# Kernel optimization log

Measured on AMD Instinct MI355X. Metric: run time of the kernel, lower is better.

## Reference

```python
import jax, jax.numpy as jnp
import numpy as np

BS = 16     # block_size
KS = 2      # kernel_size
ST = 2      # stride
TOL = 0.5   # mask threshold (avgpool=False -> max-pool reduce)


def setup_inputs() -> dict:
    key = jax.random.key(0)
    k1, k2, k3, k4 = jax.random.split(key, 4)
    inputs = jax.random.normal(k1, (8, 256, 256, 64), dtype=jnp.float32)
    mask = jax.random.uniform(k2, (8, 256, 256, 1), dtype=jnp.float32)
    # TF conv2d_transpose filter layout: [kh, kw, out_channels(filters), in_channels]
    kernel = jax.random.normal(k3, (KS, KS, 64, 64), dtype=jnp.float32) * 0.05
    bias = jax.random.normal(k4, (64,), dtype=jnp.float32) * 0.05
    return {"inputs": inputs, "mask": mask, "kernel": kernel, "bias": bias}


def reference(inputs, mask, kernel, bias):
    N, H, W, C = inputs.shape
    kh, kw, F, _ = kernel.shape
    nbh, nbw = H // BS, W // BS           # block_count
    obs = (BS - 1) * ST + kh              # output_block_size (VALID deconv of a block) = 32

    # sparse.reduce_mask: max-pool mask over each 16x16 block, threshold at tol.
    active = mask.reshape(N, nbh, BS, nbw, BS, -1).max(axis=(2, 4, 5)) > TOL  # [N, nbh, nbw]

    # sparse.gather: extract all blocks (inactive ones are masked out after the conv,
    # which reproduces scatter-into-zeros of only the active blocks).
    blocks = (inputs.reshape(N, nbh, BS, nbw, BS, C)
              .transpose(0, 1, 3, 2, 4, 5)
              .reshape(N * nbh * nbw, BS, BS, C))

    # tf.nn.conv2d_transpose (VALID, stride ST) == dilated conv with rot180 kernel.
    # kernel [kh,kw,out,in] -> HWIO [kh,kw,in,out], spatially flipped.
    w = kernel.transpose(0, 1, 3, 2)[::-1, ::-1]
    out = jax.lax.conv_general_dilated(
        blocks, w,
        window_strides=(1, 1),
        padding=[(kh - 1, kh - 1), (kw - 1, kw - 1)],
        lhs_dilation=(ST, ST),
        dimension_numbers=('NHWC', 'HWIO', 'NHWC'))  # [NB, obs, obs, F]

    out = out + bias  # bias_add; activation is identity (activation=None)

    # sparse.scatter: write active blocks into zero output (non-overlapping tiling).
    out = out.reshape(N, nbh, nbw, obs, obs, F)
    out = out * active[:, :, :, None, None, None].astype(out.dtype)
    out = out.transpose(0, 1, 3, 2, 4, 5).reshape(N, nbh * obs, nbw * obs, F)
    return out  # [N, H*ST, W*ST, F]
```

## Files before the change

### kernel.cpp

```cpp
#include <hip/hip_runtime.h>
#include <hip/hip_bf16.h>

typedef __attribute__((ext_vector_type(4))) float f32x4;
typedef __attribute__((ext_vector_type(8))) short s16x8;

__device__ inline unsigned cvtpk(float a, float b) {
  unsigned r;
  asm("v_cvt_pk_bf16_f32 %0, %1, %2" : "=v"(r) : "v"(a), "v"(b));
  return r;
}
__device__ inline s16x8 pack8(f32x4 a, f32x4 b) {
  union { unsigned u[4]; s16x8 v; } x;
  x.u[0] = cvtpk(a[0], a[1]); x.u[1] = cvtpk(a[2], a[3]);
  x.u[2] = cvtpk(b[0], b[1]); x.u[3] = cvtpk(b[2], b[3]);
  return x.v;
}

__device__ inline void lds_fence() {
  asm volatile("s_waitcnt lgkmcnt(0)" ::: "memory");
  __builtin_amdgcn_sched_barrier(0);
}

__global__ __launch_bounds__(256, 3)
void sparse_deconv_kernel(const float* __restrict__ in, const float* __restrict__ mask,
                          const float* __restrict__ kern, const float* __restrict__ bias,
                          float* __restrict__ out) {
  __shared__ float lds[4][2][2048];
  const int tid = threadIdx.x;
  const int w  = tid >> 6;
  const int l  = tid & 63;
  const int lm = l & 15;
  const int lg = l >> 4;
  const int r  = w & 1;
  const int ky = w >> 1;

  s16x8 wf[8][2];
#pragma unroll
  for (int m2 = 0; m2 < 8; ++m2) {
#pragma unroll
    for (int kf = 0; kf < 2; ++kf) {
      const float* p = kern + (((ky * 8 + m2) * 16 + lm) * 64 + kf * 32 + lg * 8);
      wf[m2][kf] = pack8(*(const f32x4*)p, *(const f32x4*)(p + 4));
    }
  }
  const f32x4 bias4 = *(const f32x4*)(bias + lm * 4);

  const int b  = blockIdx.x;
  const int n  = b >> 8;
  const int by = (b >> 4) & 15;
  const int bx = b & 15;

  const float* mp = mask + ((n * 256 + by * 16) * 256 + bx * 16);
  float mv = 0.0f;
#pragma unroll
  for (int i = 0; i < 4; ++i) {
    const int idx = i * 64 + l;
    mv = fmaxf(mv, mp[(idx >> 4) * 256 + (idx & 15)]);
  }
#pragma unroll
  for (int off = 32; off; off >>= 1)
    mv = fmaxf(mv, __shfl_xor(mv, off));
  const bool active = mv > 0.5f;

  const float* ibase = in + (((n * 256 + by * 16) * 256) + bx * 16 + lm) * 64 + lg * 8;
  float* oorigin = out + (((size_t)(n * 512 + by * 32)) * 512 + bx * 32) * 64;
  const int oyw = 2 * r + ky;

  if (active) {
    f32x4 tb[2][4];
#pragma unroll
    for (int q = 0; q < 2; ++q) {
      const float* p = ibase + (2 * q + r) * (256 * 64);
      tb[q][0] = *(const f32x4*)p;        tb[q][1] = *(const f32x4*)(p + 4);
      tb[q][2] = *(const f32x4*)(p + 32); tb[q][3] = *(const f32x4*)(p + 36);
    }
#pragma unroll
    for (int s = 0; s < 8; ++s) {
      const int bsel = s & 1;
      s16x8 xf0 = pack8(tb[bsel][0], tb[bsel][1]);
      s16x8 xf1 = pack8(tb[bsel][2], tb[bsel][3]);
      if (s < 6) {
        const float* p = ibase + (2 * (s + 2) + r) * (256 * 64);
        tb[bsel][0] = *(const f32x4*)p;        tb[bsel][1] = *(const f32x4*)(p + 4);
        tb[bsel][2] = *(const f32x4*)(p + 32); tb[bsel][3] = *(const f32x4*)(p + 36);
      }
      float* LB = &lds[w][bsel][0];
#pragma unroll
      for (int kx = 0; kx < 2; ++kx) {
#pragma unroll
        for (int ft = 0; ft < 4; ++ft) {
          f32x4 acc = {0.f, 0.f, 0.f, 0.f};
          acc = __builtin_amdgcn_mfma_f32_16x16x32_bf16(wf[kx * 4 + ft][0], xf0, acc, 0, 0, 0);
          acc = __builtin_amdgcn_mfma_f32_16x16x32_bf16(wf[kx * 4 + ft][1], xf1, acc, 0, 0, 0);
          const int p  = 2 * lm + kx;
          const int sl = (4 * ft + lg + p) & 15;
          *(f32x4*)(LB + p * 64 + sl * 4) = acc;
        }
      }
      lds_fence();

      const int oy = 4 * s + oyw;
      float* orow = oorigin + (size_t)oy * (512 * 64) + l * 4;
#pragma unroll
      for (int rc = 0; rc < 8; ++rc) {
        const int p  = rc * 4 + lg;
        const int sl = (lm + p) & 15;
        f32x4 v = *(const f32x4*)(LB + p * 64 + sl * 4);
        v += bias4;
        __builtin_nontemporal_store(v, (f32x4*)(orow + rc * 256));
      }
    }
  } else {
    const f32x4 z = {0.f, 0.f, 0.f, 0.f};
#pragma unroll
    for (int i = 0; i < 8; ++i) {
      float* orow = oorigin + (size_t)(w * 8 + i) * (512 * 64) + l * 4;
#pragma unroll
      for (int rc = 0; rc < 8; ++rc)
        __builtin_nontemporal_store(z, (f32x4*)(orow + rc * 256));
    }
  }
}

extern "C" void kernel_launch(void* const* d_in, const int* in_sizes, int n_in,
                              void* d_out, int out_size, void* d_ws, size_t ws_size,
                              hipStream_t stream) {
  const float* in   = (const float*)d_in[0];
  const float* mask = (const float*)d_in[1];
  const float* kern = (const float*)d_in[2];
  const float* bias = (const float*)d_in[3];
  float* out = (float*)d_out;
  dim3 grid(2048), block(256);
  hipLaunchKernelGGL(sparse_deconv_kernel, grid, block, 0, stream,
                     in, mask, kern, bias, out);
}
```

Measured before the change: 132.0 us.

## Give each wave both kernel rows to read each input row only once

```diff
diff --git a/kernel.cpp b/kernel.cpp
--- a/kernel.cpp
+++ b/kernel.cpp
@@ -21,7 +21,7 @@
   __builtin_amdgcn_sched_barrier(0);
 }
 
-__global__ __launch_bounds__(256, 3)
+__global__ __launch_bounds__(256, 2)
 void sparse_deconv_kernel(const float* __restrict__ in, const float* __restrict__ mask,
                           const float* __restrict__ kern, const float* __restrict__ bias,
                           float* __restrict__ out) {
@@ -31,18 +31,15 @@
   const int l  = tid & 63;
   const int lm = l & 15;
   const int lg = l >> 4;
-  const int r  = w & 1;
-  const int ky = w >> 1;
 
-  s16x8 wf[8][2];
+  s16x8 wf[16][2];
 #pragma unroll
-  for (int m2 = 0; m2 < 8; ++m2) {
+  for (int mt = 0; mt < 16; ++mt)
 #pragma unroll
     for (int kf = 0; kf < 2; ++kf) {
-      const float* p = kern + (((ky * 8 + m2) * 16 + lm) * 64 + kf * 32 + lg * 8);
-      wf[m2][kf] = pack8(*(const f32x4*)p, *(const f32x4*)(p + 4));
+      const float* p = kern + ((mt * 16 + lm) * 64 + kf * 32 + lg * 8);
+      wf[mt][kf] = pack8(*(const f32x4*)p, *(const f32x4*)(p + 4));
     }
-  }
   const f32x4 bias4 = *(const f32x4*)(bias + lm * 4);
 
   const int b  = blockIdx.x;
@@ -62,63 +59,67 @@
     mv = fmaxf(mv, __shfl_xor(mv, off));
   const bool active = mv > 0.5f;
 
-  const float* ibase = in + (((n * 256 + by * 16) * 256) + bx * 16 + lm) * 64 + lg * 8;
+  const float* ibase = in + (((n * 256 + by * 16 + w) * 256) + bx * 16 + lm) * 64 + lg * 8;
   float* oorigin = out + (((size_t)(n * 512 + by * 32)) * 512 + bx * 32) * 64;
-  const int oyw = 2 * r + ky;
 
   if (active) {
     f32x4 tb[2][4];
 #pragma unroll
     for (int q = 0; q < 2; ++q) {
-      const float* p = ibase + (2 * q + r) * (256 * 64);
+      const float* p = ibase + (4 * q) * (256 * 64);
       tb[q][0] = *(const f32x4*)p;        tb[q][1] = *(const f32x4*)(p + 4);
       tb[q][2] = *(const f32x4*)(p + 32); tb[q][3] = *(const f32x4*)(p + 36);
     }
 #pragma unroll
-    for (int s = 0; s < 8; ++s) {
+    for (int s = 0; s < 4; ++s) {
       const int bsel = s & 1;
       s16x8 xf0 = pack8(tb[bsel][0], tb[bsel][1]);
       s16x8 xf1 = pack8(tb[bsel][2], tb[bsel][3]);
-      if (s < 6) {
-        const float* p = ibase + (2 * (s + 2) + r) * (256 * 64);
+      if (s < 2) {
+        const float* p = ibase + (4 * (s + 2)) * (256 * 64);
         tb[bsel][0] = *(const f32x4*)p;        tb[bsel][1] = *(const f32x4*)(p + 4);
         tb[bsel][2] = *(const f32x4*)(p + 32); tb[bsel][3] = *(const f32x4*)(p + 36);
       }
-      float* LB = &lds[w][bsel][0];
 #pragma unroll
-      for (int kx = 0; kx < 2; ++kx) {
+      for (int ky = 0; ky < 2; ++ky) {
+        float* LB = &lds[w][ky][0];
 #pragma unroll
-        for (int ft = 0; ft < 4; ++ft) {
-          f32x4 acc = {0.f, 0.f, 0.f, 0.f};
-          acc = __builtin_amdgcn_mfma_f32_16x16x32_bf16(wf[kx * 4 + ft][0], xf0, acc, 0, 0, 0);
-          acc = __builtin_amdgcn_mfma_f32_16x16x32_bf16(wf[kx * 4 + ft][1], xf1, acc, 0, 0, 0);
-          const int p  = 2 * lm + kx;
-          const int sl = (4 * ft + lg + p) & 15;
-          *(f32x4*)(LB + p * 64 + sl * 4) = acc;
+        for (int kx = 0; kx < 2; ++kx)
+#pragma unroll
+          for (int ft = 0; ft < 4; ++ft) {
+            f32x4 acc = {0.f, 0.f, 0.f, 0.f};
+            acc = __builtin_amdgcn_mfma_f32_16x16x32_bf16(wf[ky * 8 + kx * 4 + ft][0], xf0, acc, 0, 0, 0);
+            acc = __builtin_amdgcn_mfma_f32_16x16x32_bf16(wf[ky * 8 + kx * 4 + ft][1], xf1, acc, 0, 0, 0);
+            const int p  = 2 * lm + kx;
+            const int sl = (4 * ft + lg + p) & 15;
+            *(f32x4*)(LB + p * 64 + sl * 4) = acc;
+          }
+        lds_fence();
+
+        const int oy = 8 * s + 2 * w + ky;
+        float* orow = oorigin + (size_t)oy * (512 * 64) + l * 4;
+#pragma unroll
+        for (int rc = 0; rc < 8; ++rc) {
+          const int p  = rc * 4 + lg;
+          const int sl = (lm + p) & 15;
+          f32x4 v = *(const f32x4*)(LB + p * 64 + sl * 4);
+          v += bias4;
+          __builtin_nontemporal_store(v, (f32x4*)(orow + rc * 256));
         }
-      }
-      lds_fence();
-
-      const int oy = 4 * s + oyw;
-      float* orow = oorigin + (size_t)oy * (512 * 64) + l * 4;
-#pragma unroll
-      for (int rc = 0; rc < 8; ++rc) {
-        const int p  = rc * 4 + lg;
-        const int sl = (lm + p) & 15;
-        f32x4 v = *(const f32x4*)(LB + p * 64 + sl * 4);
-        v += bias4;
-        __builtin_nontemporal_store(v, (f32x4*)(orow + rc * 256));
       }
     }
   } else {
     const f32x4 z = {0.f, 0.f, 0.f, 0.f};
 #pragma unroll
-    for (int i = 0; i < 8; ++i) {
-      float* orow = oorigin + (size_t)(w * 8 + i) * (512 * 64) + l * 4;
+    for (int s = 0; s < 4; ++s)
 #pragma unroll
-      for (int rc = 0; rc < 8; ++rc)
-        __builtin_nontemporal_store(z, (f32x4*)(orow + rc * 256));
-    }
+      for (int ky = 0; ky < 2; ++ky) {
+        const int oy = 8 * s + 2 * w + ky;
+        float* orow = oorigin + (size_t)oy * (512 * 64) + l * 4;
+#pragma unroll
+        for (int rc = 0; rc < 8; ++rc)
+          __builtin_nontemporal_store(z, (f32x4*)(orow + rc * 256));
+      }
   }
 }
 
```

Result: no change. 133.5 us (+1.1%).
